# Kernel optimization log

Measured on AMD Instinct MI355X. Metric: run time of the kernel, lower is better.

The kernel has to match this reference:

```python
import jax, jax.numpy as jnp
import numpy as np

H = 12     # attention heads
W1S = 256  # one-sided sliding window (attention_window = 512)
NW = 8     # n_windows -> global tokens at each window start


def ln(x, g, b, eps=1e-5):
    m = jnp.mean(x, -1, keepdims=True)
    v = jnp.mean(jnp.square(x - m), -1, keepdims=True)
    return (x - m) * jax.lax.rsqrt(v + eps) * g + b


def _forward(x, x_mask, word_emb, pos_emb, emb_g, emb_b, Wq, bq, Wk, bk, Wv, bv, Wo, bo,
             Wqg, bqg, Wkg, bkg, Wvg, bvg, ln1_g, ln1_b, W1, b1, W2, b2, ln2_g, ln2_b,
             out_w, out_b):
    B, S = x.shape
    D = word_emb.shape[1]
    Dh = D // H
    w = W1S
    nb = S // w
    win_len = S // NW
    g = NW
    gpos = jnp.arange(g) * win_len
    scale = 1.0 / np.sqrt(Dh)

    x_mask = x_mask.at[:, gpos].set(1)  # module forces global slots to be valid
    kmask = x_mask > 0
    is_glob = jnp.zeros((S,), bool).at[gpos].set(True)

    h = ln(word_emb[x] + pos_emb[None], emb_g, emb_b)

    # static masks for the banded (sliding-window) scores
    kidx = jnp.arange(nb)[:, None] * w + jnp.arange(3 * w)[None, :] - w  # [nb,3w] abs key idx
    in_rng = (kidx >= 0) & (kidx < S)
    kidx_c = jnp.clip(kidx, 0, S - 1)
    key_ok = in_rng[None] & kmask[:, kidx_c] & (~is_glob[kidx_c])[None]   # [B,nb,3w]
    diff = jnp.arange(3 * w)[None, :] - w - jnp.arange(w)[:, None]        # [w,3w] key-query offset
    band_mask = ((jnp.abs(diff) <= w)[None, None] & key_ok[:, :, None, :]).reshape(B, 1, S, 3 * w)
    gkey_mask = kmask[:, gpos][:, None, None, :]                           # [B,1,1,g]
    mask_all = jnp.concatenate([jnp.broadcast_to(gkey_mask, (B, 1, S, g)),
                                jnp.broadcast_to(band_mask, (B, 1, S, 3 * w))], -1)

    def heads(t):
        return t.reshape(B, S, H, Dh).transpose(0, 2, 1, 3)

    def chunk3(t):  # [B,H,S,Dh] -> [B,H,nb,3w,Dh]; block n covers key offsets [-w, 2w)
        tp = jnp.pad(t, ((0, 0), (0, 0), (w, w), (0, 0))).reshape(B, H, nb + 2, w, Dh)
        return jnp.concatenate([tp[:, :, :nb], tp[:, :, 1:nb + 1], tp[:, :, 2:]], axis=3)

    def layer(h, p):
        (wq, bq_, wk, bk_, wv, bv_, wo, bo_, wqg, bqg_, wkg, bkg_, wvg, bvg_,
         g1, gb1, w1, fb1, w2, fb2, g2, gb2) = p
        q = heads(h @ wq + bq_); k = heads(h @ wk + bk_); v = heads(h @ wv + bv_)
        # sliding-window band scores + extra global-key columns, joint softmax
        sb = jnp.einsum('bhnqd,bhnkd->bhnqk', q.reshape(B, H, nb, w, Dh), chunk3(k)) * scale
        sg = jnp.einsum('bhsd,bhgd->bhsg', q, k[:, :, gpos]) * scale
        scores = jnp.concatenate([sg, sb.reshape(B, H, S, 3 * w)], -1)
        neg = jnp.finfo(scores.dtype).min * 0.5
        probs = jax.nn.softmax(jnp.where(mask_all, scores, neg), -1)
        ctx = (jnp.einsum('bhnqk,bhnkd->bhnqd', probs[..., g:].reshape(B, H, nb, w, 3 * w), chunk3(v)).reshape(B, H, S, Dh)
               + jnp.einsum('bhsg,bhgd->bhsd', probs[..., :g], v[:, :, gpos]))
        ctx = ctx.transpose(0, 2, 1, 3).reshape(B, S, D)
        # global-token queries: full attention over all keys with separate projections
        qg = (h[:, gpos] @ wqg + bqg_).reshape(B, g, H, Dh).transpose(0, 2, 1, 3)
        kg = heads(h @ wkg + bkg_); vg = heads(h @ wvg + bvg_)
        sgl = jnp.where(kmask[:, None, None, :], jnp.einsum('bhgd,bhsd->bhgs', qg, kg) * scale, neg)
        ctxg = jnp.einsum('bhgs,bhsd->bhgd', jax.nn.softmax(sgl, -1), vg).transpose(0, 2, 1, 3).reshape(B, g, D)
        ctx = ctx.at[:, gpos].set(ctxg)
        h = ln(h + ctx @ wo + bo_, g1, gb1)
        h = ln(h + jax.nn.gelu(h @ w1 + fb1, approximate=False) @ w2 + fb2, g2, gb2)
        return h, None

    params = (Wq, bq, Wk, bk, Wv, bv, Wo, bo, Wqg, bqg, Wkg, bkg, Wvg, bvg,
              ln1_g, ln1_b, W1, b1, W2, b2, ln2_g, ln2_b)
    h, _ = jax.lax.scan(jax.checkpoint(layer), h, params)
    y = h.reshape(B * NW, win_len, D)[:, 0]   # CLS pooling per window
    return y @ out_w + out_b


def setup_inputs():
    key = jax.random.key(0)
    V, S, D, L, F, O, B = 50265, 4096, 768, 12, 3072, 128, 1
    ks = iter(jax.random.split(key, 40))
    def nrm(shape):
        return (jax.random.normal(next(ks), shape) * 0.02).astype(jnp.float32)
    inp = {
        'x': jax.random.randint(next(ks), (B, S), 0, V, dtype=jnp.int32),
        'x_mask': jnp.ones((B, S), jnp.int32),
        'word_emb': nrm((V, D)), 'pos_emb': nrm((S, D)),
        'emb_g': jnp.ones((D,)), 'emb_b': jnp.zeros((D,)),
        'Wq': nrm((L, D, D)), 'bq': jnp.zeros((L, D)),
        'Wk': nrm((L, D, D)), 'bk': jnp.zeros((L, D)),
        'Wv': nrm((L, D, D)), 'bv': jnp.zeros((L, D)),
        'Wo': nrm((L, D, D)), 'bo': jnp.zeros((L, D)),
        'Wqg': nrm((L, D, D)), 'bqg': jnp.zeros((L, D)),
        'Wkg': nrm((L, D, D)), 'bkg': jnp.zeros((L, D)),
        'Wvg': nrm((L, D, D)), 'bvg': jnp.zeros((L, D)),
        'ln1_g': jnp.ones((L, D)), 'ln1_b': jnp.zeros((L, D)),
        'W1': nrm((L, D, F)), 'b1': jnp.zeros((L, F)),
        'W2': nrm((L, F, D)), 'b2': jnp.zeros((L, D)),
        'ln2_g': jnp.ones((L, D)), 'ln2_b': jnp.zeros((L, D)),
        'out_w': nrm((D, O)), 'out_b': jnp.zeros((O,)),
    }
    return inp


def reference(x, x_mask, word_emb, pos_emb, emb_g, emb_b, Wq, bq, Wk, bk, Wv, bv, Wo, bo,
              Wqg, bqg, Wkg, bkg, Wvg, bvg, ln1_g, ln1_b, W1, b1, W2, b2, ln2_g, ln2_b,
              out_w, out_b):
    return _forward(x, x_mask, word_emb, pos_emb, emb_g, emb_b, Wq, bq, Wk, bk, Wv, bv,
                    Wo, bo, Wqg, bqg, Wkg, bkg, Wvg, bvg, ln1_g, ln1_b, W1, b1, W2, b2,
                    ln2_g, ln2_b, out_w, out_b)
```

## Files before the change

### kernel.cpp

```cpp
#include <hip/hip_runtime.h>
#include <cstddef>

#define S_LEN   4096
#define DMODEL  768
#define NHEAD   12
#define DHEAD   64
#define FDIM    3072
#define NLAYER  12
#define WIN     256
#define NGLOB   8
#define GSTRIDE 512

typedef short bf16x8 __attribute__((ext_vector_type(8)));
typedef float f32x4 __attribute__((ext_vector_type(4)));
typedef unsigned short u16;

__device__ __forceinline__ u16 f2bf(float f) {
  unsigned u = __builtin_bit_cast(unsigned, f);
  return (u16)((u + 0x7FFFu + ((u >> 16) & 1u)) >> 16);
}
__device__ __forceinline__ float bf2f(u16 s) {
  unsigned u = ((unsigned)s) << 16;
  return __builtin_bit_cast(float, u);
}

__device__ __forceinline__ void gload16(const void* g, void* l) {
  __builtin_amdgcn_global_load_lds(
      (const __attribute__((address_space(1))) void*)g,
      (__attribute__((address_space(3))) void*)l, 16, 0, 0);
}

__device__ __forceinline__ float wave_sum(float v) {
#pragma unroll
  for (int off = 32; off > 0; off >>= 1) v += __shfl_xor(v, off);
  return v;
}

__device__ __forceinline__ float block_sum256(float v, float* sbuf) {
  v = wave_sum(v);
  int w = threadIdx.x >> 6;
  __syncthreads();
  if ((threadIdx.x & 63) == 0) sbuf[w] = v;
  __syncthreads();
  return sbuf[0] + sbuf[1] + sbuf[2] + sbuf[3];
}

__global__ __launch_bounds__(256) void embed_ln_kernel(
    const int* __restrict__ x, const float* __restrict__ wemb,
    const float* __restrict__ pemb, const float* __restrict__ gg,
    const float* __restrict__ bb, float* __restrict__ h, u16* __restrict__ hb) {
  __shared__ float sbuf[4];
  int s = blockIdx.x, tid = threadIdx.x;
  int idx = x[s];
  float vals[3];
#pragma unroll
  for (int i = 0; i < 3; i++) {
    int d = tid + i * 256;
    vals[i] = wemb[(size_t)idx * DMODEL + d] + pemb[(size_t)s * DMODEL + d];
  }
  float mean = block_sum256(vals[0] + vals[1] + vals[2], sbuf) * (1.0f / 768.0f);
  float sq = 0.f;
#pragma unroll
  for (int i = 0; i < 3; i++) { float t = vals[i] - mean; sq += t * t; }
  float inv = rsqrtf(block_sum256(sq, sbuf) * (1.0f / 768.0f) + 1e-5f);
#pragma unroll
  for (int i = 0; i < 3; i++) {
    int d = tid + i * 256;
    float r = (vals[i] - mean) * inv * gg[d] + bb[d];
    h[(size_t)s * DMODEL + d] = r;
    hb[(size_t)s * DMODEL + d] = f2bf(r);
  }
}

__global__ __launch_bounds__(256) void add_ln_kernel(
    float* __restrict__ h, const u16* __restrict__ r,
    const float* __restrict__ gg, const float* __restrict__ bb,
    u16* __restrict__ hb) {
  __shared__ float sbuf[4];
  int s = blockIdx.x, tid = threadIdx.x;
  float vals[3];
#pragma unroll
  for (int i = 0; i < 3; i++) {
    int d = tid + i * 256;
    vals[i] = h[(size_t)s * DMODEL + d] + bf2f(r[(size_t)s * DMODEL + d]);
  }
  float mean = block_sum256(vals[0] + vals[1] + vals[2], sbuf) * (1.0f / 768.0f);
  float sq = 0.f;
#pragma unroll
  for (int i = 0; i < 3; i++) { float t = vals[i] - mean; sq += t * t; }
  float inv = rsqrtf(block_sum256(sq, sbuf) * (1.0f / 768.0f) + 1e-5f);
#pragma unroll
  for (int i = 0; i < 3; i++) {
    int d = tid + i * 256;
    float rr = (vals[i] - mean) * inv * gg[d] + bb[d];
    h[(size_t)s * DMODEL + d] = rr;
    hb[(size_t)s * DMODEL + d] = f2bf(rr);
  }
}

#define DD_ ((size_t)DMODEL * DMODEL)
#define DF_ ((size_t)DMODEL * FDIM)
#define WSTRIDE (6 * DD_ + 2 * DF_)
__global__ __launch_bounds__(256) void convw_kernel(
    const float* __restrict__ Wq, const float* __restrict__ Wk,
    const float* __restrict__ Wv, const float* __restrict__ Wkg,
    const float* __restrict__ Wvg, const float* __restrict__ Wo,
    const float* __restrict__ W1, const float* __restrict__ W2,
    u16* __restrict__ wt) {
  int l = blockIdx.y;
  int bid = blockIdx.x;
  const float* src; u16* dst; int K, N, r;
  u16* base = wt + (size_t)l * WSTRIDE;
  if (bid < 864) {
    int m = bid / 144; r = bid % 144; K = 768; N = 768;
    switch (m) {
      case 0: src = Wq  + l * DD_; dst = base;           break;
      case 1: src = Wk  + l * DD_; dst = base + 1 * DD_; break;
      case 2: src = Wv  + l * DD_; dst = base + 2 * DD_; break;
      case 3: src = Wkg + l * DD_; dst = base + 3 * DD_; break;
      case 4: src = Wvg + l * DD_; dst = base + 4 * DD_; break;
      default: src = Wo + l * DD_; dst = base + 5 * DD_; break;
    }
  } else if (bid < 1440) {
    r = bid - 864; K = 768; N = 3072; src = W1 + l * DF_; dst = base + 6 * DD_;
  } else {
    r = bid - 1440; K = 3072; N = 768; src = W2 + l * DF_; dst = base + 6 * DD_ + DF_;
  }
  int nt = N / 64;
  int tk = (r / nt) * 64, tn = (r % nt) * 64;
  int t = threadIdx.x;
  int c = t >> 2, ko = t & 3;
#pragma unroll
  for (int p = 0; p < 2; p++) {
    int kb = (p * 4 + ko) * 8;
    const float* sp = src + (size_t)(tk + kb) * N + tn + c;
    bf16x8 val;
#pragma unroll
    for (int j = 0; j < 8; j++) val[j] = (short)f2bf(sp[(size_t)j * N]);
    *(bf16x8*)&dst[(size_t)(tn + c) * K + tk + kb] = val;
  }
}

template <int ACT, int OUTM, int TM>
__device__ __forceinline__ void mm_core(const u16* __restrict__ A, const u16* __restrict__ Wt,
                                        const float* __restrict__ bias, void* __restrict__ Cv,
                                        int M, int N, int K, int bm, int bn,
                                        u16* As, u16* Bs) {
  constexpr int MR = TM / 32;
  constexpr int AJ = TM / 32;
  int t = threadIdx.x;
  int wid = t >> 6, lane = t & 63;
  int wr = (wid >> 1) * (TM / 2), wc = (wid & 1) * 64;
  int lr = lane & 15, lg = lane >> 4;
  f32x4 acc[MR][4];
  f32x4 zf = {0.f, 0.f, 0.f, 0.f};
#pragma unroll
  for (int m = 0; m < MR; m++)
#pragma unroll
    for (int n = 0; n < 4; n++) acc[m][n] = zf;

  int srow = wid * 8 + (lane >> 3);
  int sgr = (lane & 7) ^ (lane >> 3);
  const u16* aSrc = A + (size_t)(bm + srow) * K + sgr * 8;
  const u16* bSrc = Wt + (size_t)(bn + srow) * K + sgr * 8;
  int dstOff = wid * 8 * 64;

  for (int kt = 0; kt < K; kt += 64) {
    __syncthreads();
#pragma unroll
    for (int j = 0; j < AJ; j++)
      gload16(aSrc + kt + (size_t)j * 32 * K, As + dstOff + j * 32 * 64);
#pragma unroll
    for (int j = 0; j < 4; j++)
      gload16(bSrc + kt + (size_t)j * 32 * K, Bs + dstOff + j * 32 * 64);
    __syncthreads();
#pragma unroll
    for (int ks = 0; ks < 2; ks++) {
      bf16x8 af[MR], bfr[4];
#pragma unroll
      for (int m = 0; m < MR; m++)
        af[m] = *(const bf16x8*)&As[(wr + m * 16 + lr) * 64 + (((ks * 4 + lg) ^ (lr & 7)) * 8)];
#pragma unroll
      for (int n = 0; n < 4; n++)
        bfr[n] = *(const bf16x8*)&Bs[(wc + n * 16 + lr) * 64 + (((ks * 4 + lg) ^ (lr & 7)) * 8)];
#pragma unroll
      for (int m = 0; m < MR; m++)
#pragma unroll
        for (int n = 0; n < 4; n++)
          acc[m][n] = __builtin_amdgcn_mfma_f32_16x16x32_bf16(af[m], bfr[n], acc[m][n], 0, 0, 0);
    }
  }
#pragma unroll
  for (int n = 0; n < 4; n++) {
    int col = bn + wc + n * 16 + lr;
    float bb = bias[col];
#pragma unroll
    for (int m = 0; m < MR; m++) {
#pragma unroll
      for (int r = 0; r < 4; r++) {
        int row = bm + wr + m * 16 + lg * 4 + r;
        float xv = acc[m][n][r] + bb;
        if (ACT == 1) xv = 0.5f * xv * (1.0f + erff(xv * 0.70710678118654752f));
        if (OUTM == 0) ((float*)Cv)[(size_t)row * N + col] = xv;
        else if (OUTM == 1) ((u16*)Cv)[(size_t)row * N + col] = f2bf(xv);
        else ((u16*)Cv)[(size_t)col * M + row] = f2bf(xv);
      }
    }
  }
}

template <int ACT, int OUTM, int TM>
__global__ __launch_bounds__(256) void mm_kernel(const u16* A, const u16* Wt, const float* bias,
                                                 void* Cv, int M, int N, int K) {
  __shared__ u16 As[TM * 64];
  __shared__ u16 Bs[128 * 64];
  int nwg = gridDim.x * gridDim.y;
  int lin = blockIdx.y * gridDim.x + blockIdx.x;
  int swz = (lin & 7) * (nwg >> 3) + (lin >> 3);
  int bx = swz / gridDim.y, by = swz % gridDim.y;
  mm_core<ACT, OUTM, TM>(A, Wt, bias, Cv, M, N, K, by * TM, bx * 128, As, Bs);
}

__global__ __launch_bounds__(256) void mm5_kernel(
    const u16* A,
    const u16* W0, const u16* W1_, const u16* W2_, const u16* W3, const u16* W4,
    const float* b0, const float* b1, const float* b2, const float* b3, const float* b4,
    u16* C0, u16* C1, u16* C2, u16* C3, u16* C4, int M, int K,
    const float* __restrict__ h, const float* __restrict__ Wqg,
    const float* __restrict__ bqg, float* __restrict__ qg) {
  __shared__ u16 As[128 * 64];
  __shared__ u16 Bs[128 * 64];
  if (blockIdx.x == 30) {
    int b = blockIdx.y;
    if (b >= 24) return;
    int gi = b / 3, c0 = (b % 3) * 256;
    int tid = threadIdx.x;
    float* hs = (float*)As;
    const float* hrow = h + (size_t)gi * GSTRIDE * DMODEL;
    for (int i = tid; i < DMODEL; i += 256) hs[i] = hrow[i];
    __syncthreads();
    float a = bqg[c0 + tid];
    for (int k = 0; k < DMODEL; k++) a += hs[k] * Wqg[(size_t)k * DMODEL + c0 + tid];
    qg[gi * DMODEL + c0 + tid] = a;
    return;
  }
  int lin = blockIdx.y * 30 + blockIdx.x;
  int swz = (lin & 7) * 120 + (lin >> 3);
  int bx = swz >> 5, by = swz & 31;
  int which = bx / 6;
  int bn = (bx % 6) * 128;
  const u16* Ws[5] = {W0, W1_, W2_, W3, W4};
  const float* bs[5] = {b0, b1, b2, b3, b4};
  u16* Cs[5] = {C0, C1, C2, C3, C4};
  if (which == 2 || which == 4)
    mm_core<0, 2, 128>(A, Ws[which], bs[which], Cs[which], M, DMODEL, K, by * 128, bn, As, Bs);
  else
    mm_core<0, 1, 128>(A, Ws[which], bs[which], Cs[which], M, DMODEL, K, by * 128, bn, As, Bs);
}

__device__ __forceinline__ void sliding_body(
    int bid, u16* Ps,
    const u16* __restrict__ qb, const u16* __restrict__ kb,
    const u16* __restrict__ vt, const int* __restrict__ xmask,
    u16* __restrict__ ctx) {
  int hh = bid >> 5;
  int q0 = (bid & 31) * 128;
  int w = threadIdx.x >> 6, lane = threadIdx.x & 63;
  int lr = lane & 15, lg = lane >> 4;
  int rowb = q0 + w * 32;
  f32x4 zf = {0.f, 0.f, 0.f, 0.f};
  u16* Pw = Ps + w * 2048;

  bf16x8 qf[2][2];
#pragma unroll
  for (int mf = 0; mf < 2; mf++) {
    const u16* qptr = qb + (size_t)(rowb + mf * 16 + lr) * DMODEL + hh * DHEAD;
    qf[mf][0] = *(const bf16x8*)(qptr + lg * 8);
    qf[mf][1] = *(const bf16x8*)(qptr + 32 + lg * 8);
  }

  float m_run[2][4], l_run[2][4];
  f32x4 ctxa[2][4];
#pragma unroll
  for (int mf = 0; mf < 2; mf++)
#pragma unroll
    for (int r = 0; r < 4; r++) {
      m_run[mf][r] = -1e30f; l_run[mf][r] = 0.f; ctxa[mf][r] = zf;
    }

  {
    int krow = (lr < NGLOB) ? lr * GSTRIDE : 0;
    const u16* kp = kb + (size_t)krow * DMODEL + hh * DHEAD + lg * 8;
    bf16x8 kf0 = *(const bf16x8*)kp;
    bf16x8 kf1 = *(const bf16x8*)(kp + 32);
#pragma unroll
    for (int mf = 0; mf < 2; mf++) {
      f32x4 sa = __builtin_amdgcn_mfma_f32_16x16x32_bf16(qf[mf][0], kf0, zf, 0, 0, 0);
      sa = __builtin_amdgcn_mfma_f32_16x16x32_bf16(qf[mf][1], kf1, sa, 0, 0, 0);
      float p0[4], tmax[4];
#pragma unroll
      for (int r = 0; r < 4; r++) {
        float s = (lr < NGLOB) ? sa[r] * 0.125f : -1e30f;
        p0[r] = s; tmax[r] = s;
      }
#pragma unroll
      for (int o = 8; o; o >>= 1)
#pragma unroll
        for (int r = 0; r < 4; r++) tmax[r] = fmaxf(tmax[r], __shfl_xor(tmax[r], o));
      float tsum[4];
#pragma unroll
      for (int r = 0; r < 4; r++) {
        m_run[mf][r] = tmax[r];
        p0[r] = __expf(p0[r] - tmax[r]);
        tsum[r] = p0[r];
      }
#pragma unroll
      for (int o = 8; o; o >>= 1)
#pragma unroll
        for (int r = 0; r < 4; r++) tsum[r] += __shfl_xor(tsum[r], o);
#pragma unroll
      for (int r = 0; r < 4; r++) l_run[mf][r] = tsum[r];
#pragma unroll
      for (int r = 0; r < 4; r++) {
        int qi = mf * 16 + lg * 4 + r;
        Pw[qi * 64 + (((lr >> 3) ^ (qi & 7)) * 8) + (lr & 7)] = f2bf(p0[r]);
        int k2 = 16 + lr;
        Pw[qi * 64 + (((k2 >> 3) ^ (qi & 7)) * 8) + (k2 & 7)] = 0;
      }
    }
    bf16x8 pf0 = *(const bf16x8*)&Pw[lr * 64 + ((lg ^ (lr & 7)) * 8)];
    bf16x8 pf1 = *(const bf16x8*)&Pw[(16 + lr) * 64 + ((lg ^ (lr & 7)) * 8)];
#pragma unroll
    for (int c2 = 0; c2 < 4; c2++) {
      bf16x8 vg8 = {0, 0, 0, 0, 0, 0, 0, 0};
      if (lg == 0) {
        const u16* vrow = vt + (size_t)(hh * DHEAD + c2 * 16 + lr) * S_LEN;
#pragma unroll
        for (int j = 0; j < 8; j++) vg8[j] = (short)vrow[(size_t)j * GSTRIDE];
      }
      ctxa[0][c2] = __builtin_amdgcn_mfma_f32_16x16x32_bf16(pf0, vg8, ctxa[0][c2], 0, 0, 0);
      ctxa[1][c2] = __builtin_amdgcn_mfma_f32_16x16x32_bf16(pf1, vg8, ctxa[1][c2], 0, 0, 0);
    }
  }

  for (int tt = 0; tt < 10; tt++) {
    int base = q0 - WIN + tt * 64;
    if (base + 63 < 0 || base >= S_LEN) continue;
    bf16x8 kf[4][2];
    int keyc[4]; bool vc[4];
#pragma unroll
    for (int c = 0; c < 4; c++) {
      int key = base + c * 16 + lr;
      int krow = key < 0 ? 0 : (key > S_LEN - 1 ? S_LEN - 1 : key);
      vc[c] = (key >= 0) && (key < S_LEN) && ((key & (GSTRIDE - 1)) != 0) && (xmask[krow] != 0);
      keyc[c] = key;
      const u16* kp = kb + (size_t)krow * DMODEL + hh * DHEAD + lg * 8;
      kf[c][0] = *(const bf16x8*)kp;
      kf[c][1] = *(const bf16x8*)(kp + 32);
    }
#pragma unroll
    for (int mf = 0; mf < 2; mf++) {
      f32x4 sa[4];
#pragma unroll
      for (int c = 0; c < 4; c++) {
        sa[c] = __builtin_amdgcn_mfma_f32_16x16x32_bf16(qf[mf][0], kf[c][0], zf, 0, 0, 0);
        sa[c] = __builtin_amdgcn_mfma_f32_16x16x32_bf16(qf[mf][1], kf[c][1], sa[c], 0, 0, 0);
      }
      float p[4][4], tmax[4] = {-1e30f, -1e30f, -1e30f, -1e30f};
#pragma unroll
      for (int c = 0; c < 4; c++)
#pragma unroll
        for (int r = 0; r < 4; r++) {
          int qrow = rowb + mf * 16 + lg * 4 + r;
          int dd = keyc[c] - qrow;
          float s = (vc[c] && dd >= -WIN && dd <= WIN) ? sa[c][r] * 0.125f : -1e30f;
          p[c][r] = s;
          tmax[r] = fmaxf(tmax[r], s);
        }
#pragma unroll
      for (int o = 8; o; o >>= 1)
#pragma unroll
        for (int r = 0; r < 4; r++) tmax[r] = fmaxf(tmax[r], __shfl_xor(tmax[r], o));
      float sc[4], tsum[4] = {0.f, 0.f, 0.f, 0.f};
#pragma unroll
      for (int r = 0; r < 4; r++) {
        float mn = fmaxf(m_run[mf][r], tmax[r]);
        sc[r] = __expf(m_run[mf][r] - mn);
        m_run[mf][r] = mn;
      }
#pragma unroll
      for (int c = 0; c < 4; c++)
#pragma unroll
        for (int r = 0; r < 4; r++) {
          p[c][r] = __expf(p[c][r] - m_run[mf][r]);
          tsum[r] += p[c][r];
        }
#pragma unroll
      for (int o = 8; o; o >>= 1)
#pragma unroll
        for (int r = 0; r < 4; r++) tsum[r] += __shfl_xor(tsum[r], o);
#pragma unroll
      for (int r = 0; r < 4; r++) l_run[mf][r] = l_run[mf][r] * sc[r] + tsum[r];
#pragma unroll
      for (int c2 = 0; c2 < 4; c2++)
#pragma unroll
        for (int r = 0; r < 4; r++) ctxa[mf][c2][r] *= sc[r];
#pragma unroll
      for (int c = 0; c < 4; c++)
#pragma unroll
        for (int r = 0; r < 4; r++) {
          int qi = mf * 16 + lg * 4 + r, k64 = c * 16 + lr;
          Pw[qi * 64 + (((k64 >> 3) ^ (qi & 7)) * 8) + (k64 & 7)] = f2bf(p[c][r]);
        }
    }
#pragma unroll
    for (int ks = 0; ks < 2; ks++) {
      bf16x8 pf0 = *(const bf16x8*)&Pw[lr * 64 + (((ks * 4 + lg) ^ (lr & 7)) * 8)];
      bf16x8 pf1 = *(const bf16x8*)&Pw[(16 + lr) * 64 + (((ks * 4 + lg) ^ (lr & 7)) * 8)];
      int kstart = base + ks * 32 + lg * 8;
      int kc = kstart < 0 ? 0 : (kstart > S_LEN - 8 ? S_LEN - 8 : kstart);
#pragma unroll
      for (int c2 = 0; c2 < 4; c2++) {
        const u16* vp = vt + (size_t)(hh * DHEAD + c2 * 16 + lr) * S_LEN + kc;
        bf16x8 vf = *(const bf16x8*)vp;
        ctxa[0][c2] = __builtin_amdgcn_mfma_f32_16x16x32_bf16(pf0, vf, ctxa[0][c2], 0, 0, 0);
        ctxa[1][c2] = __builtin_amdgcn_mfma_f32_16x16x32_bf16(pf1, vf, ctxa[1][c2], 0, 0, 0);
      }
    }
  }

#pragma unroll
  for (int mf = 0; mf < 2; mf++)
#pragma unroll
    for (int c2 = 0; c2 < 4; c2++)
#pragma unroll
      for (int r = 0; r < 4; r++) {
        int qrow = rowb + mf * 16 + lg * 4 + r;
        if ((qrow & (GSTRIDE - 1)) != 0)
          ctx[(size_t)qrow * DMODEL + hh * DHEAD + c2 * 16 + lr] = f2bf(ctxa[mf][c2][r] / l_run[mf][r]);
      }
}

__device__ __forceinline__ void gattn_body(
    int hh, u16* Ps, float* cM, float* cL, float* cA,
    const float* __restrict__ qg, const u16* __restrict__ kg,
    const u16* __restrict__ vgt, const int* __restrict__ xmask,
    u16* __restrict__ ctx) {
  int w = threadIdx.x >> 6, lane = threadIdx.x & 63;
  int lr = lane & 15, lg = lane >> 4;
  f32x4 zf = {0.f, 0.f, 0.f, 0.f};
  u16* Pw = Ps + w * 1024;

  bf16x8 qf0, qf1;
  {
    const float* qp = qg + (size_t)(lr & 7) * DMODEL + hh * DHEAD;
    bool real = lr < 8;
#pragma unroll
    for (int j = 0; j < 8; j++) {
      qf0[j] = real ? (short)f2bf(0.125f * qp[lg * 8 + j]) : (short)0;
      qf1[j] = real ? (short)f2bf(0.125f * qp[32 + lg * 8 + j]) : (short)0;
    }
  }

  float m_run[4] = {-1e30f, -1e30f, -1e30f, -1e30f};
  float l_run[4] = {0.f, 0.f, 0.f, 0.f};
  f32x4 ctxa[4] = {zf, zf, zf, zf};

  for (int tt = w; tt < 64; tt += 4) {
    int base = tt * 64;
    f32x4 sa[4];
    bool vc[4];
#pragma unroll
    for (int st = 0; st < 4; st++) {
      int key = base + st * 16 + lr;
      vc[st] = (xmask[key] != 0) || ((key & (GSTRIDE - 1)) == 0);
      const u16* kp = kg + (size_t)key * DMODEL + hh * DHEAD + lg * 8;
      sa[st] = __builtin_amdgcn_mfma_f32_16x16x32_bf16(qf0, *(const bf16x8*)kp, zf, 0, 0, 0);
      sa[st] = __builtin_amdgcn_mfma_f32_16x16x32_bf16(qf1, *(const bf16x8*)(kp + 32), sa[st], 0, 0, 0);
    }
    float p[4][4], tmax[4] = {-1e30f, -1e30f, -1e30f, -1e30f};
#pragma unroll
    for (int st = 0; st < 4; st++)
#pragma unroll
      for (int r = 0; r < 4; r++) {
        float s = vc[st] ? sa[st][r] : -1e30f;
        p[st][r] = s;
        tmax[r] = fmaxf(tmax[r], s);
      }
#pragma unroll
    for (int o = 8; o; o >>= 1)
#pragma unroll
      for (int r = 0; r < 4; r++) tmax[r] = fmaxf(tmax[r], __shfl_xor(tmax[r], o));
    float sc[4], tsum[4] = {0.f, 0.f, 0.f, 0.f};
#pragma unroll
    for (int r = 0; r < 4; r++) {
      float mn = fmaxf(m_run[r], tmax[r]);
      sc[r] = __expf(m_run[r] - mn);
      m_run[r] = mn;
    }
#pragma unroll
    for (int st = 0; st < 4; st++)
#pragma unroll
      for (int r = 0; r < 4; r++) {
        float pv = vc[st] ? __expf(p[st][r] - m_run[r]) : 0.f;
        p[st][r] = pv;
        tsum[r] += pv;
      }
#pragma unroll
    for (int o = 8; o; o >>= 1)
#pragma unroll
      for (int r = 0; r < 4; r++) tsum[r] += __shfl_xor(tsum[r], o);
#pragma unroll
    for (int r = 0; r < 4; r++) l_run[r] = l_run[r] * sc[r] + tsum[r];
#pragma unroll
    for (int c2 = 0; c2 < 4; c2++)
#pragma unroll
      for (int r = 0; r < 4; r++) ctxa[c2][r] *= sc[r];
#pragma unroll
    for (int st = 0; st < 4; st++)
#pragma unroll
      for (int r = 0; r < 4; r++) {
        int qi = lg * 4 + r, k64 = st * 16 + lr;
        Pw[qi * 64 + (((k64 >> 3) ^ (qi & 7)) * 8) + (k64 & 7)] = f2bf(p[st][r]);
      }
#pragma unroll
    for (int ks = 0; ks < 2; ks++) {
      bf16x8 pf = *(const bf16x8*)&Pw[lr * 64 + (((ks * 4 + lg) ^ (lr & 7)) * 8)];
      int kstart = base + ks * 32 + lg * 8;
#pragma unroll
      for (int c2 = 0; c2 < 4; c2++) {
        const u16* vp = vgt + (size_t)(hh * DHEAD + c2 * 16 + lr) * S_LEN + kstart;
        ctxa[c2] = __builtin_amdgcn_mfma_f32_16x16x32_bf16(pf, *(const bf16x8*)vp, ctxa[c2], 0, 0, 0);
      }
    }
  }

  if (lg < 2) {
#pragma unroll
    for (int r = 0; r < 4; r++) {
      int q = lg * 4 + r;
#pragma unroll
      for (int c2 = 0; c2 < 4; c2++)
        cA[(w * 8 + q) * 64 + c2 * 16 + lr] = ctxa[c2][r];
      if (lr == 0) {
        cM[w * 8 + q] = m_run[r];
        cL[w * 8 + q] = l_run[r];
      }
    }
  }
  __syncthreads();
  int t = threadIdx.x;
#pragma unroll
  for (int half = 0; half < 2; half++) {
    int slot = half * 256 + t;
    int q = slot >> 6, d = slot & 63;
    float M = fmaxf(fmaxf(cM[q], cM[8 + q]), fmaxf(cM[16 + q], cM[24 + q]));
    float L = 0.f, A = 0.f;
#pragma unroll
    for (int ww = 0; ww < 4; ww++) {
      float al = __expf(cM[ww * 8 + q] - M);
      L += cL[ww * 8 + q] * al;
      A += cA[(ww * 8 + q) * 64 + d] * al;
    }
    ctx[(size_t)q * GSTRIDE * DMODEL + hh * DHEAD + d] = f2bf(A / L);
  }
}

__global__ __launch_bounds__(256) void attn_kernel(
    const u16* __restrict__ qb, const u16* __restrict__ kb,
    const u16* __restrict__ vt, const int* __restrict__ xmask,
    u16* __restrict__ ctx,
    const float* __restrict__ qg, const u16* __restrict__ kg,
    const u16* __restrict__ vgt) {
  __shared__ u16 Ps[4 * 32 * 64];
  __shared__ float cM[32], cL[32], cA[32 * 64];
  int bid = blockIdx.x;
  if (bid < NHEAD) {
    gattn_body(bid, Ps, cM, cL, cA, qg, kg, vgt, xmask, ctx);
  } else {
    sliding_body(bid - NHEAD, Ps, qb, kb, vt, xmask, ctx);
  }
}

__global__ __launch_bounds__(128) void cls_out_kernel(
    const float* __restrict__ h, const float* __restrict__ ow,
    const float* __restrict__ ob, float* __restrict__ y) {
  __shared__ float hs[DMODEL];
  int wi = blockIdx.x;
  int tid = threadIdx.x;
  for (int i = tid; i < DMODEL; i += 128) hs[i] = h[(size_t)wi * GSTRIDE * DMODEL + i];
  __syncthreads();
  float a = ob[tid];
  for (int d = 0; d < DMODEL; d++) a += hs[d] * ow[d * 128 + tid];
  y[wi * 128 + tid] = a;
}

extern "C" void kernel_launch(void* const* d_in, const int* in_sizes, int n_in,
                              void* d_out, int out_size, void* d_ws, size_t ws_size,
                              hipStream_t stream) {
  const int*   x      = (const int*)d_in[0];
  const int*   xmask  = (const int*)d_in[1];
  const float* wemb   = (const float*)d_in[2];
  const float* pemb   = (const float*)d_in[3];
  const float* emb_g  = (const float*)d_in[4];
  const float* emb_b  = (const float*)d_in[5];
  const float* Wq     = (const float*)d_in[6];
  const float* bq     = (const float*)d_in[7];
  const float* Wk     = (const float*)d_in[8];
  const float* bk     = (const float*)d_in[9];
  const float* Wv     = (const float*)d_in[10];
  const float* bv     = (const float*)d_in[11];
  const float* Wo     = (const float*)d_in[12];
  const float* bo     = (const float*)d_in[13];
  const float* Wqg    = (const float*)d_in[14];
  const float* bqg    = (const float*)d_in[15];
  const float* Wkg    = (const float*)d_in[16];
  const float* bkg    = (const float*)d_in[17];
  const float* Wvg    = (const float*)d_in[18];
  const float* bvg    = (const float*)d_in[19];
  const float* ln1_g  = (const float*)d_in[20];
  const float* ln1_b  = (const float*)d_in[21];
  const float* W1     = (const float*)d_in[22];
  const float* b1     = (const float*)d_in[23];
  const float* W2     = (const float*)d_in[24];
  const float* b2     = (const float*)d_in[25];
  const float* ln2_g  = (const float*)d_in[26];
  const float* ln2_b  = (const float*)d_in[27];
  const float* out_w  = (const float*)d_in[28];
  const float* out_b  = (const float*)d_in[29];

  char* wsp = (char*)d_ws;
  float* h   = (float*)wsp;  wsp += (size_t)S_LEN * DMODEL * 4;
  u16* tmpb  = (u16*)wsp;    wsp += (size_t)S_LEN * DMODEL * 2;
  u16* hb  = (u16*)wsp;      wsp += (size_t)S_LEN * DMODEL * 2;
  u16* ctx = (u16*)wsp;      wsp += (size_t)S_LEN * DMODEL * 2;
  u16* qb  = (u16*)wsp;      wsp += (size_t)S_LEN * DMODEL * 2;
  u16* kb  = (u16*)wsp;      wsp += (size_t)S_LEN * DMODEL * 2;
  u16* vt  = (u16*)wsp;      wsp += (size_t)S_LEN * DMODEL * 2;
  u16* kgb = (u16*)wsp;      wsp += (size_t)S_LEN * DMODEL * 2;
  u16* vgt = (u16*)wsp;      wsp += (size_t)S_LEN * DMODEL * 2;
  u16* mid = (u16*)wsp;      wsp += (size_t)S_LEN * FDIM * 2;
  float* qgb = (float*)wsp;  wsp += (size_t)NGLOB * DMODEL * 4;
  u16* wtb = (u16*)wsp;      wsp += WSTRIDE * NLAYER * 2;

  embed_ln_kernel<<<S_LEN, 256, 0, stream>>>(x, wemb, pemb, emb_g, emb_b, h, hb);
  convw_kernel<<<dim3(2016, NLAYER), 256, 0, stream>>>(Wq, Wk, Wv, Wkg, Wvg, Wo, W1, W2, wtb);

  for (int l = 0; l < NLAYER; l++) {
    const float* bql  = bq  + (size_t)l * DMODEL;
    const float* bkl  = bk  + (size_t)l * DMODEL;
    const float* bvl  = bv  + (size_t)l * DMODEL;
    const float* bol  = bo  + (size_t)l * DMODEL;
    const float* wqg  = Wqg + (size_t)l * DD_;
    const float* bqgl = bqg + (size_t)l * DMODEL;
    const float* bkgl = bkg + (size_t)l * DMODEL;
    const float* bvgl = bvg + (size_t)l * DMODEL;
    const float* b1l  = b1  + (size_t)l * FDIM;
    const float* b2l  = b2  + (size_t)l * DMODEL;
    u16* base = wtb + (size_t)l * WSTRIDE;
    u16* wqT  = base;
    u16* wkT  = base + 1 * DD_;
    u16* wvT  = base + 2 * DD_;
    u16* wkgT = base + 3 * DD_;
    u16* wvgT = base + 4 * DD_;
    u16* woT  = base + 5 * DD_;
    u16* w1T  = base + 6 * DD_;
    u16* w2T  = base + 6 * DD_ + DF_;

    mm5_kernel<<<dim3(31, 32), 256, 0, stream>>>(
        hb, wqT, wkT, wvT, wkgT, wvgT, bql, bkl, bvl, bkgl, bvgl,
        qb, kb, vt, kgb, vgt, S_LEN, DMODEL, h, wqg, bqgl, qgb);

    attn_kernel<<<NHEAD + NHEAD * 32, 256, 0, stream>>>(
        qb, kb, vt, xmask, ctx, qgb, kgb, vgt);

    mm_kernel<0, 1, 64><<<dim3(6, 64), 256, 0, stream>>>(ctx, woT, bol, tmpb, S_LEN, DMODEL, DMODEL);
    add_ln_kernel<<<S_LEN, 256, 0, stream>>>(h, tmpb, ln1_g + (size_t)l * DMODEL,
                                             ln1_b + (size_t)l * DMODEL, hb);

    mm_kernel<1, 1, 128><<<dim3(24, 32), 256, 0, stream>>>(hb, w1T, b1l, mid, S_LEN, FDIM, DMODEL);
    mm_kernel<0, 1, 64><<<dim3(6, 64), 256, 0, stream>>>(mid, w2T, b2l, tmpb, S_LEN, DMODEL, FDIM);
    add_ln_kernel<<<S_LEN, 256, 0, stream>>>(h, tmpb, ln2_g + (size_t)l * DMODEL,
                                             ln2_b + (size_t)l * DMODEL, hb);
  }

  cls_out_kernel<<<NGLOB, 128, 0, stream>>>(h, out_w, out_b, (float*)d_out);
}
```

Baseline: 2.945 ms.

## Double-buffer GEMM LDS tiles with K-step 32 to overlap loads and MFMA

Reworks the shared GEMM core to stage 32-wide K slices into two LDS buffers, issuing the next slice's global-to-LDS load before computing on the current one. This removes the per-iteration barrier stall between loading and computing, at the same LDS footprint. It halves the K depth per step, so there are twice as many barriers and fewer MFMAs between them, and the swizzle changes to a 4-group XOR pattern.

```diff
diff --git a/kernel.cpp b/kernel.cpp
--- a/kernel.cpp
+++ b/kernel.cpp
@@ -147,7 +147,9 @@
                                         int M, int N, int K, int bm, int bn,
                                         u16* As, u16* Bs) {
   constexpr int MR = TM / 32;
-  constexpr int AJ = TM / 32;
+  constexpr int AJ = TM / 64;
+  constexpr int ATS = TM * 32;
+  constexpr int BTS = 128 * 32;
   int t = threadIdx.x;
   int wid = t >> 6, lane = t & 63;
   int wr = (wid >> 1) * (TM / 2), wc = (wid & 1) * 64;
@@ -159,36 +161,46 @@
 #pragma unroll
     for (int n = 0; n < 4; n++) acc[m][n] = zf;
 
-  int srow = wid * 8 + (lane >> 3);
-  int sgr = (lane & 7) ^ (lane >> 3);
-  const u16* aSrc = A + (size_t)(bm + srow) * K + sgr * 8;
-  const u16* bSrc = Wt + (size_t)(bn + srow) * K + sgr * 8;
-  int dstOff = wid * 8 * 64;
-
-  for (int kt = 0; kt < K; kt += 64) {
+  int lrow = lane >> 2;
+  int sgr = (lane & 3) ^ (lrow & 3);
+  const u16* aSrc = A + (size_t)(bm + wid * (AJ * 16) + lrow) * K + sgr * 8;
+  const u16* bSrc = Wt + (size_t)(bn + wid * 32 + lrow) * K + sgr * 8;
+
+  auto STAGE = [&](int kt, int buf) {
+#pragma unroll
+    for (int j = 0; j < AJ; j++)
+      gload16(aSrc + kt * 32 + (size_t)j * 16 * K,
+              As + buf * ATS + (wid * AJ * 16 + j * 16) * 32);
+#pragma unroll
+    for (int j = 0; j < 2; j++)
+      gload16(bSrc + kt * 32 + (size_t)j * 16 * K,
+              Bs + buf * BTS + (wid * 32 + j * 16) * 32);
+  };
+
+  int nk = K >> 5;
+  STAGE(0, 0);
+  __syncthreads();
+  int cur = 0;
+  for (int kt = 0; kt < nk; kt++) {
+    if (kt + 1 < nk) STAGE(kt + 1, cur ^ 1);
+    bf16x8 af[MR], bfr[4];
+#pragma unroll
+    for (int m = 0; m < MR; m++) {
+      int row = wr + m * 16 + lr;
+      af[m] = *(const bf16x8*)&As[cur * ATS + row * 32 + ((lg ^ (lr & 3)) * 8)];
+    }
+#pragma unroll
+    for (int n = 0; n < 4; n++) {
+      int row = wc + n * 16 + lr;
+      bfr[n] = *(const bf16x8*)&Bs[cur * BTS + row * 32 + ((lg ^ (lr & 3)) * 8)];
+    }
+#pragma unroll
+    for (int m = 0; m < MR; m++)
+#pragma unroll
+      for (int n = 0; n < 4; n++)
+        acc[m][n] = __builtin_amdgcn_mfma_f32_16x16x32_bf16(af[m], bfr[n], acc[m][n], 0, 0, 0);
     __syncthreads();
-#pragma unroll
-    for (int j = 0; j < AJ; j++)
-      gload16(aSrc + kt + (size_t)j * 32 * K, As + dstOff + j * 32 * 64);
-#pragma unroll
-    for (int j = 0; j < 4; j++)
-      gload16(bSrc + kt + (size_t)j * 32 * K, Bs + dstOff + j * 32 * 64);
-    __syncthreads();
-#pragma unroll
-    for (int ks = 0; ks < 2; ks++) {
-      bf16x8 af[MR], bfr[4];
-#pragma unroll
-      for (int m = 0; m < MR; m++)
-        af[m] = *(const bf16x8*)&As[(wr + m * 16 + lr) * 64 + (((ks * 4 + lg) ^ (lr & 7)) * 8)];
-#pragma unroll
-      for (int n = 0; n < 4; n++)
-        bfr[n] = *(const bf16x8*)&Bs[(wc + n * 16 + lr) * 64 + (((ks * 4 + lg) ^ (lr & 7)) * 8)];
-#pragma unroll
-      for (int m = 0; m < MR; m++)
-#pragma unroll
-        for (int n = 0; n < 4; n++)
-          acc[m][n] = __builtin_amdgcn_mfma_f32_16x16x32_bf16(af[m], bfr[n], acc[m][n], 0, 0, 0);
-    }
+    cur ^= 1;
   }
 #pragma unroll
   for (int n = 0; n < 4; n++) {
@@ -212,8 +224,8 @@
 template <int ACT, int OUTM, int TM>
 __global__ __launch_bounds__(256) void mm_kernel(const u16* A, const u16* Wt, const float* bias,
                                                  void* Cv, int M, int N, int K) {
-  __shared__ u16 As[TM * 64];
-  __shared__ u16 Bs[128 * 64];
+  __shared__ u16 As[2 * TM * 32];
+  __shared__ u16 Bs[2 * 128 * 32];
   int nwg = gridDim.x * gridDim.y;
   int lin = blockIdx.y * gridDim.x + blockIdx.x;
   int swz = (lin & 7) * (nwg >> 3) + (lin >> 3);
@@ -228,8 +240,8 @@
     u16* C0, u16* C1, u16* C2, u16* C3, u16* C4, int M, int K,
     const float* __restrict__ h, const float* __restrict__ Wqg,
     const float* __restrict__ bqg, float* __restrict__ qg) {
-  __shared__ u16 As[128 * 64];
-  __shared__ u16 Bs[128 * 64];
+  __shared__ u16 As[2 * 128 * 32];
+  __shared__ u16 Bs[2 * 128 * 32];
   if (blockIdx.x == 30) {
     int b = blockIdx.y;
     if (b >= 24) return;
```

New measurement: 3.106 ms. 5.5% more time.
